# Kernel optimization log

Hardware: AMD Instinct MI355X
Metric: run time of the kernel (lower is better)

## Reference

```python
import jax, jax.numpy as jnp
import numpy as np

B, S, D = 1, 2048, 2048
H, DH, DHID, DKER = 16, 128, 128, 64
EPS = 1e-6

def _gelu(x):
    return jax.nn.gelu(x, approximate=False)  # torch F.gelu default is exact erf

def setup_inputs() -> dict:
    key = jax.random.key(0)
    ks = jax.random.split(key, 12)
    inp = {
        'q': jax.random.normal(ks[0], (B, S, D), jnp.float32),
        'k': jax.random.normal(ks[1], (B, S, D), jnp.float32),
        'v': jax.random.normal(ks[2], (B, S, D), jnp.float32),
        'lr_attn_mask': jax.random.randint(ks[3], (1, 1, S, S), 0, 2) > 0,
        'sparse_norms_lse': jax.random.normal(ks[4], (B, H, S, 1), jnp.float32),
        'sparse_attn_weights': jax.random.normal(ks[5], (B, H, S, S), jnp.float32) * 0.1,
        'kernel_q_mat1': jax.random.normal(ks[6], (H, DH, DHID), jnp.float32) * 0.05,
        'kernel_k_mat1': jax.random.normal(ks[7], (H, DH, DHID), jnp.float32) * 0.05,
        'kernel_q_mat2': jax.random.normal(ks[8], (H, DHID, DKER), jnp.float32) * 0.05,
        'kernel_k_mat2': jax.random.normal(ks[9], (H, DHID, DKER), jnp.float32) * 0.05,
        'interaction_k': jax.random.normal(ks[10], (H, DKER, DKER), jnp.float32) * 0.05,
        'scalingD': jnp.ones((1, H, 1, DKER), jnp.float32) * 1e-4,
        'scalingD2': jnp.ones((1, H, 1, DKER), jnp.float32) * 1e-4,
    }
    return inp

def reference(q, k, v, lr_attn_mask, sparse_norms_lse, sparse_attn_weights,
              kernel_q_mat1, kernel_k_mat1, kernel_q_mat2, kernel_k_mat2,
              interaction_k, scalingD, scalingD2):
    b, s, d = q.shape
    dh = d // H
    # [B,S,D] -> [B,H,S,dh]
    q = q.reshape(b, s, H, dh).transpose(0, 2, 1, 3)
    k = k.reshape(b, s, H, dh).transpose(0, 2, 1, 3)
    v = v.reshape(b, s, H, dh).transpose(0, 2, 1, 3)
    # per-head kernel feature maps (dropout is identity, p=0.0)
    q = _gelu(jnp.einsum('bhsd,hde->bhse', q, kernel_q_mat1))
    q = _gelu(jnp.einsum('bhsd,hde->bhse', q, kernel_q_mat2))
    k = _gelu(jnp.einsum('bhsd,hde->bhse', k, kernel_k_mat1))
    k = jnp.abs(scalingD) * _gelu(jnp.einsum('bhsd,hde->bhse', k, kernel_k_mat2))
    k = k + jnp.einsum('bhse,hef->bhsf', k, interaction_k) * scalingD2
    # low-rank kernelized scores: [B,H,S,S]
    out = jnp.einsum('bhse,bhte->bhst', jnp.abs(q), jnp.abs(k))
    mask = lr_attn_mask  # bool, broadcasts over [B,H,S,S]
    out = jnp.where(mask, out, 0.0)
    lr_norms_lse = jnp.log(out.sum(axis=-1, keepdims=True) + EPS)
    norm_factor_lse = jnp.logaddexp(lr_norms_lse, sparse_norms_lse)
    # log-domain merge of low-rank and sparse scores
    out = jnp.where(mask, jnp.log(out + EPS), sparse_attn_weights)
    out = jnp.exp(out - norm_factor_lse)
    out = jnp.einsum('bhst,bhtd->bhsd', out, v)
    return out.transpose(0, 2, 1, 3).reshape(b, s, d)
```

## Files before the change

kernel.cpp:

```cpp
#include <hip/hip_runtime.h>
#include <math.h>

#define S 2048
#define DD 2048
#define NH 16
#define DH 128
#define DHID 128
#define DKER 64
#define EPSF 1e-6f

typedef __attribute__((ext_vector_type(8))) short bf16x8;
typedef __attribute__((ext_vector_type(4))) float f32x4;

__device__ __forceinline__ float gelu_f(float x) {
    return 0.5f * x * (1.0f + erff(x * 0.7071067811865475f));
}

__device__ __forceinline__ ushort f2b(float x) {
    uint32_t u = __float_as_uint(x);
    uint32_t r = (u + 0x7FFFu + ((u >> 16) & 1u)) >> 16;
    return (ushort)r;
}

__global__ __launch_bounds__(256) void k_mlp1(const float* __restrict__ X,
                                              const float* __restrict__ Wall,
                                              float* __restrict__ Y) {
    const int h = blockIdx.y;
    const int s0 = blockIdx.x * 64;
    const int tid = threadIdx.x;
    const int ty = tid >> 4, tx = tid & 15;
    __shared__ float Xs[64][20];
    __shared__ float Ws[16][128];
    const float* Wh = Wall + h * DH * DHID;
    float acc[4][8] = {};

    const int lr = tid >> 2, lc = tid & 3;
    const int wr = tid >> 5, wc = tid & 31;
    for (int kc = 0; kc < 8; ++kc) {
        *(float4*)(&Xs[lr][lc * 4]) =
            *(const float4*)(X + (size_t)(s0 + lr) * DD + h * DH + kc * 16 + lc * 4);
        *(float4*)(&Ws[wr][wc * 4]) =
            *(const float4*)(Wh + (kc * 16 + wr) * DHID + wc * 4);
        *(float4*)(&Ws[wr + 8][wc * 4]) =
            *(const float4*)(Wh + (kc * 16 + wr + 8) * DHID + wc * 4);
        __syncthreads();
        #pragma unroll
        for (int kk = 0; kk < 16; ++kk) {
            float a[4];
            #pragma unroll
            for (int i = 0; i < 4; ++i) a[i] = Xs[ty * 4 + i][kk];
            float4 b0 = *(const float4*)(&Ws[kk][tx * 8]);
            float4 b1 = *(const float4*)(&Ws[kk][tx * 8 + 4]);
            #pragma unroll
            for (int i = 0; i < 4; ++i) {
                acc[i][0] += a[i] * b0.x; acc[i][1] += a[i] * b0.y;
                acc[i][2] += a[i] * b0.z; acc[i][3] += a[i] * b0.w;
                acc[i][4] += a[i] * b1.x; acc[i][5] += a[i] * b1.y;
                acc[i][6] += a[i] * b1.z; acc[i][7] += a[i] * b1.w;
            }
        }
        __syncthreads();
    }
    float* Yp = Y + ((size_t)h * S + s0) * DHID;
    #pragma unroll
    for (int i = 0; i < 4; ++i) {
        float4 o0, o1;
        o0.x = gelu_f(acc[i][0]); o0.y = gelu_f(acc[i][1]);
        o0.z = gelu_f(acc[i][2]); o0.w = gelu_f(acc[i][3]);
        o1.x = gelu_f(acc[i][4]); o1.y = gelu_f(acc[i][5]);
        o1.z = gelu_f(acc[i][6]); o1.w = gelu_f(acc[i][7]);
        *(float4*)(Yp + (ty * 4 + i) * DHID + tx * 8) = o0;
        *(float4*)(Yp + (ty * 4 + i) * DHID + tx * 8 + 4) = o1;
    }
}

__global__ __launch_bounds__(256) void k_mlp2_q(const float* __restrict__ Y1,
                                                const float* __restrict__ Wall,
                                                ushort* __restrict__ Q2) {
    const int h = blockIdx.y;
    const int s0 = blockIdx.x * 64;
    const int tid = threadIdx.x;
    const int ty = tid >> 4, tx = tid & 15;
    __shared__ float Ys[64][20];
    __shared__ float Ws[16][64];
    const float* Wh = Wall + h * DHID * DKER;
    float acc[4][4] = {};
    const int lr = tid >> 2, lc = tid & 3;
    const int wr = tid >> 4, wc = tid & 15;
    for (int kc = 0; kc < 8; ++kc) {
        *(float4*)(&Ys[lr][lc * 4]) =
            *(const float4*)(Y1 + ((size_t)h * S + s0 + lr) * DHID + kc * 16 + lc * 4);
        *(float4*)(&Ws[wr][wc * 4]) =
            *(const float4*)(Wh + (kc * 16 + wr) * DKER + wc * 4);
        __syncthreads();
        #pragma unroll
        for (int kk = 0; kk < 16; ++kk) {
            float4 b = *(const float4*)(&Ws[kk][tx * 4]);
            #pragma unroll
            for (int i = 0; i < 4; ++i) {
                float a = Ys[ty * 4 + i][kk];
                acc[i][0] += a * b.x; acc[i][1] += a * b.y;
                acc[i][2] += a * b.z; acc[i][3] += a * b.w;
            }
        }
        __syncthreads();
    }
    ushort* Qp = Q2 + ((size_t)h * S + s0) * DKER;
    #pragma unroll
    for (int i = 0; i < 4; ++i) {
        ushort4 o;
        o.x = f2b(fabsf(gelu_f(acc[i][0]))); o.y = f2b(fabsf(gelu_f(acc[i][1])));
        o.z = f2b(fabsf(gelu_f(acc[i][2]))); o.w = f2b(fabsf(gelu_f(acc[i][3])));
        *(ushort4*)(Qp + (ty * 4 + i) * DKER + tx * 4) = o;
    }
}

__global__ __launch_bounds__(256) void k_mlp2_k(const float* __restrict__ Y1,
                                                const float* __restrict__ Wall,
                                                const float* __restrict__ Ikall,
                                                const float* __restrict__ sD,
                                                const float* __restrict__ sD2,
                                                ushort* __restrict__ K3) {
    const int h = blockIdx.y;
    const int s0 = blockIdx.x * 64;
    const int tid = threadIdx.x;
    const int ty = tid >> 4, tx = tid & 15;
    __shared__ float Ys[64][20];
    __shared__ float Ws[16][64];
    __shared__ float K2s[64][68];
    __shared__ float Iks[64][64];
    const float* Wh = Wall + h * DHID * DKER;
    const float* Ikh = Ikall + h * DKER * DKER;
    #pragma unroll
    for (int it = 0; it < 4; ++it) {
        int idx = it * 256 + tid;
        int r = idx >> 4, c = idx & 15;
        *(float4*)(&Iks[r][c * 4]) = *(const float4*)(Ikh + r * DKER + c * 4);
    }
    float acc[4][4] = {};
    const int lr = tid >> 2, lc = tid & 3;
    const int wr = tid >> 4, wc = tid & 15;
    for (int kc = 0; kc < 8; ++kc) {
        *(float4*)(&Ys[lr][lc * 4]) =
            *(const float4*)(Y1 + ((size_t)h * S + s0 + lr) * DHID + kc * 16 + lc * 4);
        *(float4*)(&Ws[wr][wc * 4]) =
            *(const float4*)(Wh + (kc * 16 + wr) * DKER + wc * 4);
        __syncthreads();
        #pragma unroll
        for (int kk = 0; kk < 16; ++kk) {
            float4 b = *(const float4*)(&Ws[kk][tx * 4]);
            #pragma unroll
            for (int i = 0; i < 4; ++i) {
                float a = Ys[ty * 4 + i][kk];
                acc[i][0] += a * b.x; acc[i][1] += a * b.y;
                acc[i][2] += a * b.z; acc[i][3] += a * b.w;
            }
        }
        __syncthreads();
    }
    float sdv[4], sd2v[4];
    #pragma unroll
    for (int j = 0; j < 4; ++j) {
        sdv[j] = fabsf(sD[h * DKER + tx * 4 + j]);
        sd2v[j] = sD2[h * DKER + tx * 4 + j];
    }
    float k2r[4][4];
    #pragma unroll
    for (int i = 0; i < 4; ++i) {
        #pragma unroll
        for (int j = 0; j < 4; ++j) k2r[i][j] = sdv[j] * gelu_f(acc[i][j]);
        float4 o; o.x = k2r[i][0]; o.y = k2r[i][1]; o.z = k2r[i][2]; o.w = k2r[i][3];
        *(float4*)(&K2s[ty * 4 + i][tx * 4]) = o;
    }
    __syncthreads();
    float acc2[4][4] = {};
    #pragma unroll 16
    for (int f = 0; f < 64; ++f) {
        float4 b = *(const float4*)(&Iks[f][tx * 4]);
        #pragma unroll
        for (int i = 0; i < 4; ++i) {
            float a = K2s[ty * 4 + i][f];
            acc2[i][0] += a * b.x; acc2[i][1] += a * b.y;
            acc2[i][2] += a * b.z; acc2[i][3] += a * b.w;
        }
    }
    ushort* Kp = K3 + ((size_t)h * S + s0) * DKER;
    #pragma unroll
    for (int i = 0; i < 4; ++i) {
        ushort4 o;
        o.x = f2b(fabsf(k2r[i][0] + acc2[i][0] * sd2v[0]));
        o.y = f2b(fabsf(k2r[i][1] + acc2[i][1] * sd2v[1]));
        o.z = f2b(fabsf(k2r[i][2] + acc2[i][2] * sd2v[2]));
        o.w = f2b(fabsf(k2r[i][3] + acc2[i][3] * sd2v[3]));
        *(ushort4*)(Kp + (ty * 4 + i) * DKER + tx * 4) = o;
    }
}

__global__ __launch_bounds__(256) void k_vt(const float* __restrict__ V,
                                            ushort* __restrict__ Vt) {
    const int h = blockIdx.y;
    const int t0 = blockIdx.x * 64;
    const int tid = threadIdx.x;
    __shared__ ushort Ls[128][72];
    #pragma unroll
    for (int it = 0; it < 8; ++it) {
        int idx = it * 256 + tid;
        int r = idx >> 5, c4 = idx & 31;
        float4 v = *(const float4*)(V + (size_t)(t0 + r) * DD + h * DH + c4 * 4);
        Ls[c4 * 4 + 0][r] = f2b(v.x);
        Ls[c4 * 4 + 1][r] = f2b(v.y);
        Ls[c4 * 4 + 2][r] = f2b(v.z);
        Ls[c4 * 4 + 3][r] = f2b(v.w);
    }
    __syncthreads();
    #pragma unroll
    for (int it = 0; it < 4; ++it) {
        int idx = it * 256 + tid;
        int row = idx >> 3, cc = idx & 7;
        *(bf16x8*)(Vt + ((size_t)h * DH + row) * S + t0 + cc * 8) =
            *(const bf16x8*)(&Ls[row][cc * 8]);
    }
}

__global__ __launch_bounds__(256) void k_attn(const ushort* __restrict__ Q2,
                                              const ushort* __restrict__ K3,
                                              const ushort* __restrict__ Vt,
                                              const int* __restrict__ mask,
                                              const float* __restrict__ Wsp,
                                              const float* __restrict__ lse,
                                              float* __restrict__ out) {
    const int h = blockIdx.y;
    const int s0 = blockIdx.x * 64;
    const int tid = threadIdx.x;
    const int wv = tid >> 6;
    const int lane = tid & 63;
    const int ln = lane & 15;
    const int quad = lane >> 4;
    __shared__ ushort Q2s[64][72];
    __shared__ ushort K3s[64][72];
    __shared__ ushort Vts[128][72];
    __shared__ ushort Ps[4][16][72];

    #pragma unroll
    for (int it = 0; it < 2; ++it) {
        int idx = it * 256 + tid;
        int r = idx >> 3, c = idx & 7;
        *(bf16x8*)&Q2s[r][c * 8] =
            *(const bf16x8*)(Q2 + ((size_t)h * S + s0 + r) * DKER + c * 8);
    }

    f32x4 O[8];
    #pragma unroll
    for (int v = 0; v < 8; ++v) O[v] = (f32x4){0.f, 0.f, 0.f, 0.f};
    float rs[4] = {0.f, 0.f, 0.f, 0.f};
    const int srow_q = s0 + wv * 16 + quad * 4;

    for (int t0 = 0; t0 < S; t0 += 64) {
        __syncthreads();
        #pragma unroll
        for (int it = 0; it < 2; ++it) {
            int idx = it * 256 + tid;
            int r = idx >> 3, c = idx & 7;
            *(bf16x8*)&K3s[r][c * 8] =
                *(const bf16x8*)(K3 + ((size_t)h * S + t0 + r) * DKER + c * 8);
        }
        #pragma unroll
        for (int it = 0; it < 4; ++it) {
            int idx = it * 256 + tid;
            int r = idx >> 3, c = idx & 7;
            *(bf16x8*)&Vts[r][c * 8] =
                *(const bf16x8*)(Vt + ((size_t)h * DH + r) * S + t0 + c * 8);
        }
        int mk[4][4];
        float ww[4][4];
        #pragma unroll
        for (int n = 0; n < 4; ++n)
            #pragma unroll
            for (int r = 0; r < 4; ++r) {
                size_t off = (size_t)(srow_q + r) * S + t0 + n * 16 + ln;
                mk[n][r] = mask[off];
                ww[n][r] = Wsp[(size_t)h * S * S + off];
            }
        __syncthreads();

        f32x4 sc[4];
        #pragma unroll
        for (int n = 0; n < 4; ++n) sc[n] = (f32x4){0.f, 0.f, 0.f, 0.f};
        #pragma unroll
        for (int ks = 0; ks < 2; ++ks) {
            bf16x8 af = *(const bf16x8*)&Q2s[wv * 16 + ln][ks * 32 + quad * 8];
            #pragma unroll
            for (int n = 0; n < 4; ++n) {
                bf16x8 bf = *(const bf16x8*)&K3s[n * 16 + ln][ks * 32 + quad * 8];
                sc[n] = __builtin_amdgcn_mfma_f32_16x16x32_bf16(af, bf, sc[n], 0, 0, 0);
            }
        }
        #pragma unroll
        for (int n = 0; n < 4; ++n)
            #pragma unroll
            for (int r = 0; r < 4; ++r) {
                float s = sc[n][r];
                float p;
                if (mk[n][r]) { rs[r] += s; p = s + EPSF; }
                else          { p = expf(ww[n][r]); }
                Ps[wv][quad * 4 + r][n * 16 + ln] = f2b(p);
            }
        #pragma unroll
        for (int ks = 0; ks < 2; ++ks) {
            bf16x8 pf = *(const bf16x8*)&Ps[wv][ln][ks * 32 + quad * 8];
            #pragma unroll
            for (int v = 0; v < 8; ++v) {
                bf16x8 vf = *(const bf16x8*)&Vts[v * 16 + ln][ks * 32 + quad * 8];
                O[v] = __builtin_amdgcn_mfma_f32_16x16x32_bf16(pf, vf, O[v], 0, 0, 0);
            }
        }
    }
    #pragma unroll
    for (int r = 0; r < 4; ++r) {
        float v = rs[r];
        v += __shfl_xor(v, 1); v += __shfl_xor(v, 2);
        v += __shfl_xor(v, 4); v += __shfl_xor(v, 8);
        rs[r] = v;
    }
    float idv[4];
    #pragma unroll
    for (int r = 0; r < 4; ++r)
        idv[r] = 1.f / (rs[r] + EPSF + expf(lse[(size_t)h * S + srow_q + r]));
    #pragma unroll
    for (int v = 0; v < 8; ++v)
        #pragma unroll
        for (int r = 0; r < 4; ++r)
            out[(size_t)(srow_q + r) * DD + h * DH + v * 16 + ln] = O[v][r] * idv[r];
}

extern "C" void kernel_launch(void* const* d_in, const int* in_sizes, int n_in,
                              void* d_out, int out_size, void* d_ws, size_t ws_size,
                              hipStream_t stream) {
    const float* q   = (const float*)d_in[0];
    const float* k   = (const float*)d_in[1];
    const float* v   = (const float*)d_in[2];
    const int*   msk = (const int*)d_in[3];
    const float* lse = (const float*)d_in[4];
    const float* spw = (const float*)d_in[5];
    const float* wq1 = (const float*)d_in[6];
    const float* wk1 = (const float*)d_in[7];
    const float* wq2 = (const float*)d_in[8];
    const float* wk2 = (const float*)d_in[9];
    const float* ik  = (const float*)d_in[10];
    const float* sD  = (const float*)d_in[11];
    const float* sD2 = (const float*)d_in[12];
    float* out = (float*)d_out;

    float* ws = (float*)d_ws;
    float*  q1  = ws;
    float*  k1  = q1 + (size_t)NH * S * DHID;
    ushort* q2b = (ushort*)(k1 + (size_t)NH * S * DHID);
    ushort* k3b = q2b + (size_t)NH * S * DKER;
    ushort* vt  = k3b + (size_t)NH * S * DKER;

    dim3 g(S / 64, NH), b(256);
    k_mlp1<<<g, b, 0, stream>>>(q, wq1, q1);
    k_mlp1<<<g, b, 0, stream>>>(k, wk1, k1);
    k_mlp2_q<<<g, b, 0, stream>>>(q1, wq2, q2b);
    k_mlp2_k<<<g, b, 0, stream>>>(k1, wk2, ik, sD, sD2, k3b);
    k_vt<<<g, b, 0, stream>>>(v, vt);
    k_attn<<<g, b, 0, stream>>>(q2b, k3b, vt, msk, spw, lse, out);
}
```

Before: 564.9 us.

## Move feature MLPs to bf16 MFMA, bit-pack mask, split attention over keys

Replaces the fp32 SIMT feature-map GEMMs with fused bf16 MFMA kernels that keep the hidden layer in LDS, using weights transposed and converted in a small prep kernel. The int32 mask is packed into bitmasks with a ballot, which cuts mask traffic in the attention loop. Attention is split in two along the key dimension to get more blocks in flight, with a combine kernel that adds the partial sums and normalises. It also switches to the fast __expf. Running the MLPs in bf16 adds rounding error, and the split writes partial outputs to a workspace buffer.

```diff
diff --git a/kernel.cpp b/kernel.cpp
--- a/kernel.cpp
+++ b/kernel.cpp
@@ -22,178 +22,192 @@
     return (ushort)r;
 }
 
-__global__ __launch_bounds__(256) void k_mlp1(const float* __restrict__ X,
-                                              const float* __restrict__ Wall,
-                                              float* __restrict__ Y) {
+__device__ __forceinline__ bf16x8 pack8(float4 a, float4 b) {
+    bf16x8 r;
+    r[0] = (short)f2b(a.x); r[1] = (short)f2b(a.y);
+    r[2] = (short)f2b(a.z); r[3] = (short)f2b(a.w);
+    r[4] = (short)f2b(b.x); r[5] = (short)f2b(b.y);
+    r[6] = (short)f2b(b.z); r[7] = (short)f2b(b.w);
+    return r;
+}
+
+__global__ __launch_bounds__(256) void k_wprep(const float* __restrict__ wq1,
+                                               const float* __restrict__ wk1,
+                                               const float* __restrict__ wq2,
+                                               const float* __restrict__ wk2,
+                                               const float* __restrict__ ik,
+                                               ushort* __restrict__ w1qt,
+                                               ushort* __restrict__ w1kt,
+                                               ushort* __restrict__ w2qt,
+                                               ushort* __restrict__ w2kt,
+                                               ushort* __restrict__ ikt) {
+    const int h = blockIdx.x, m = blockIdx.y, tid = threadIdx.x;
+    const float* src; ushort* dst; int E, D;
+    if (m == 0)      { src = wq1 + h * 16384; dst = w1qt + h * 16384; E = 128; D = 128; }
+    else if (m == 1) { src = wk1 + h * 16384; dst = w1kt + h * 16384; E = 128; D = 128; }
+    else if (m == 2) { src = wq2 + h * 8192;  dst = w2qt + h * 8192;  E = 64;  D = 128; }
+    else if (m == 3) { src = wk2 + h * 8192;  dst = w2kt + h * 8192;  E = 64;  D = 128; }
+    else             { src = ik  + h * 4096;  dst = ikt  + h * 4096;  E = 64;  D = 64;  }
+    const int dsh = (D == 128) ? 7 : 6;
+    const int n = E * D;
+    for (int idx = tid; idx < n; idx += 256) {
+        int e = idx >> dsh, d = idx & (D - 1);
+        dst[idx] = f2b(src[d * E + e]);
+    }
+}
+
+__global__ __launch_bounds__(256) void k_fq(const float* __restrict__ X,
+                                            const ushort* __restrict__ w1t,
+                                            const ushort* __restrict__ w2t,
+                                            ushort* __restrict__ Q2) {
     const int h = blockIdx.y;
     const int s0 = blockIdx.x * 64;
     const int tid = threadIdx.x;
-    const int ty = tid >> 4, tx = tid & 15;
-    __shared__ float Xs[64][20];
-    __shared__ float Ws[16][128];
-    const float* Wh = Wall + h * DH * DHID;
-    float acc[4][8] = {};
-
-    const int lr = tid >> 2, lc = tid & 3;
-    const int wr = tid >> 5, wc = tid & 31;
-    for (int kc = 0; kc < 8; ++kc) {
-        *(float4*)(&Xs[lr][lc * 4]) =
-            *(const float4*)(X + (size_t)(s0 + lr) * DD + h * DH + kc * 16 + lc * 4);
-        *(float4*)(&Ws[wr][wc * 4]) =
-            *(const float4*)(Wh + (kc * 16 + wr) * DHID + wc * 4);
-        *(float4*)(&Ws[wr + 8][wc * 4]) =
-            *(const float4*)(Wh + (kc * 16 + wr + 8) * DHID + wc * 4);
-        __syncthreads();
-        #pragma unroll
-        for (int kk = 0; kk < 16; ++kk) {
-            float a[4];
-            #pragma unroll
-            for (int i = 0; i < 4; ++i) a[i] = Xs[ty * 4 + i][kk];
-            float4 b0 = *(const float4*)(&Ws[kk][tx * 8]);
-            float4 b1 = *(const float4*)(&Ws[kk][tx * 8 + 4]);
-            #pragma unroll
-            for (int i = 0; i < 4; ++i) {
-                acc[i][0] += a[i] * b0.x; acc[i][1] += a[i] * b0.y;
-                acc[i][2] += a[i] * b0.z; acc[i][3] += a[i] * b0.w;
-                acc[i][4] += a[i] * b1.x; acc[i][5] += a[i] * b1.y;
-                acc[i][6] += a[i] * b1.z; acc[i][7] += a[i] * b1.w;
-            }
-        }
-        __syncthreads();
-    }
-    float* Yp = Y + ((size_t)h * S + s0) * DHID;
-    #pragma unroll
-    for (int i = 0; i < 4; ++i) {
-        float4 o0, o1;
-        o0.x = gelu_f(acc[i][0]); o0.y = gelu_f(acc[i][1]);
-        o0.z = gelu_f(acc[i][2]); o0.w = gelu_f(acc[i][3]);
-        o1.x = gelu_f(acc[i][4]); o1.y = gelu_f(acc[i][5]);
-        o1.z = gelu_f(acc[i][6]); o1.w = gelu_f(acc[i][7]);
-        *(float4*)(Yp + (ty * 4 + i) * DHID + tx * 8) = o0;
-        *(float4*)(Yp + (ty * 4 + i) * DHID + tx * 8 + 4) = o1;
-    }
-}
-
-__global__ __launch_bounds__(256) void k_mlp2_q(const float* __restrict__ Y1,
-                                                const float* __restrict__ Wall,
-                                                ushort* __restrict__ Q2) {
+    const int wv = tid >> 6, lane = tid & 63;
+    const int ln = lane & 15, quad = lane >> 4;
+    __shared__ ushort Y1s[64][136];
+
+    const float* Xr = X + (size_t)(s0 + wv * 16 + ln) * DD + h * DH;
+    bf16x8 a1[4];
+    #pragma unroll
+    for (int ks = 0; ks < 4; ++ks)
+        a1[ks] = pack8(*(const float4*)(Xr + ks * 32 + quad * 8),
+                       *(const float4*)(Xr + ks * 32 + quad * 8 + 4));
+
+    const ushort* W1h = w1t + (size_t)h * DH * DHID;
+    f32x4 c1[8];
+    #pragma unroll
+    for (int n = 0; n < 8; ++n) c1[n] = (f32x4){0.f, 0.f, 0.f, 0.f};
+    #pragma unroll
+    for (int n = 0; n < 8; ++n)
+        #pragma unroll
+        for (int ks = 0; ks < 4; ++ks) {
+            bf16x8 b = *(const bf16x8*)(W1h + (size_t)(n * 16 + ln) * DHID +
+                                        ks * 32 + quad * 8);
+            c1[n] = __builtin_amdgcn_mfma_f32_16x16x32_bf16(a1[ks], b, c1[n], 0, 0, 0);
+        }
+    #pragma unroll
+    for (int n = 0; n < 8; ++n)
+        #pragma unroll
+        for (int r = 0; r < 4; ++r)
+            Y1s[wv * 16 + quad * 4 + r][n * 16 + ln] = f2b(gelu_f(c1[n][r]));
+
+    bf16x8 a2[4];
+    #pragma unroll
+    for (int ks = 0; ks < 4; ++ks)
+        a2[ks] = *(const bf16x8*)&Y1s[wv * 16 + ln][ks * 32 + quad * 8];
+    const ushort* W2h = w2t + (size_t)h * DKER * DHID;
+    f32x4 c2[4];
+    #pragma unroll
+    for (int n = 0; n < 4; ++n) c2[n] = (f32x4){0.f, 0.f, 0.f, 0.f};
+    #pragma unroll
+    for (int n = 0; n < 4; ++n)
+        #pragma unroll
+        for (int ks = 0; ks < 4; ++ks) {
+            bf16x8 b = *(const bf16x8*)(W2h + (size_t)(n * 16 + ln) * DHID +
+                                        ks * 32 + quad * 8);
+            c2[n] = __builtin_amdgcn_mfma_f32_16x16x32_bf16(a2[ks], b, c2[n], 0, 0, 0);
+        }
+    #pragma unroll
+    for (int n = 0; n < 4; ++n)
+        #pragma unroll
+        for (int r = 0; r < 4; ++r)
+            Q2[((size_t)h * S + s0 + wv * 16 + quad * 4 + r) * DKER + n * 16 + ln] =
+                f2b(fabsf(gelu_f(c2[n][r])));
+}
+
+__global__ __launch_bounds__(256) void k_fk(const float* __restrict__ X,
+                                            const ushort* __restrict__ w1t,
+                                            const ushort* __restrict__ w2t,
+                                            const ushort* __restrict__ ikt,
+                                            const float* __restrict__ sD,
+                                            const float* __restrict__ sD2,
+                                            ushort* __restrict__ K3) {
     const int h = blockIdx.y;
     const int s0 = blockIdx.x * 64;
     const int tid = threadIdx.x;
-    const int ty = tid >> 4, tx = tid & 15;
-    __shared__ float Ys[64][20];
-    __shared__ float Ws[16][64];
-    const float* Wh = Wall + h * DHID * DKER;
-    float acc[4][4] = {};
-    const int lr = tid >> 2, lc = tid & 3;
-    const int wr = tid >> 4, wc = tid & 15;
-    for (int kc = 0; kc < 8; ++kc) {
-        *(float4*)(&Ys[lr][lc * 4]) =
-            *(const float4*)(Y1 + ((size_t)h * S + s0 + lr) * DHID + kc * 16 + lc * 4);
-        *(float4*)(&Ws[wr][wc * 4]) =
-            *(const float4*)(Wh + (kc * 16 + wr) * DKER + wc * 4);
-        __syncthreads();
-        #pragma unroll
-        for (int kk = 0; kk < 16; ++kk) {
-            float4 b = *(const float4*)(&Ws[kk][tx * 4]);
-            #pragma unroll
-            for (int i = 0; i < 4; ++i) {
-                float a = Ys[ty * 4 + i][kk];
-                acc[i][0] += a * b.x; acc[i][1] += a * b.y;
-                acc[i][2] += a * b.z; acc[i][3] += a * b.w;
-            }
-        }
-        __syncthreads();
-    }
-    ushort* Qp = Q2 + ((size_t)h * S + s0) * DKER;
-    #pragma unroll
-    for (int i = 0; i < 4; ++i) {
-        ushort4 o;
-        o.x = f2b(fabsf(gelu_f(acc[i][0]))); o.y = f2b(fabsf(gelu_f(acc[i][1])));
-        o.z = f2b(fabsf(gelu_f(acc[i][2]))); o.w = f2b(fabsf(gelu_f(acc[i][3])));
-        *(ushort4*)(Qp + (ty * 4 + i) * DKER + tx * 4) = o;
-    }
-}
-
-__global__ __launch_bounds__(256) void k_mlp2_k(const float* __restrict__ Y1,
-                                                const float* __restrict__ Wall,
-                                                const float* __restrict__ Ikall,
-                                                const float* __restrict__ sD,
-                                                const float* __restrict__ sD2,
-                                                ushort* __restrict__ K3) {
-    const int h = blockIdx.y;
-    const int s0 = blockIdx.x * 64;
-    const int tid = threadIdx.x;
-    const int ty = tid >> 4, tx = tid & 15;
-    __shared__ float Ys[64][20];
-    __shared__ float Ws[16][64];
-    __shared__ float K2s[64][68];
-    __shared__ float Iks[64][64];
-    const float* Wh = Wall + h * DHID * DKER;
-    const float* Ikh = Ikall + h * DKER * DKER;
-    #pragma unroll
-    for (int it = 0; it < 4; ++it) {
-        int idx = it * 256 + tid;
-        int r = idx >> 4, c = idx & 15;
-        *(float4*)(&Iks[r][c * 4]) = *(const float4*)(Ikh + r * DKER + c * 4);
-    }
-    float acc[4][4] = {};
-    const int lr = tid >> 2, lc = tid & 3;
-    const int wr = tid >> 4, wc = tid & 15;
-    for (int kc = 0; kc < 8; ++kc) {
-        *(float4*)(&Ys[lr][lc * 4]) =
-            *(const float4*)(Y1 + ((size_t)h * S + s0 + lr) * DHID + kc * 16 + lc * 4);
-        *(float4*)(&Ws[wr][wc * 4]) =
-            *(const float4*)(Wh + (kc * 16 + wr) * DKER + wc * 4);
-        __syncthreads();
-        #pragma unroll
-        for (int kk = 0; kk < 16; ++kk) {
-            float4 b = *(const float4*)(&Ws[kk][tx * 4]);
-            #pragma unroll
-            for (int i = 0; i < 4; ++i) {
-                float a = Ys[ty * 4 + i][kk];
-                acc[i][0] += a * b.x; acc[i][1] += a * b.y;
-                acc[i][2] += a * b.z; acc[i][3] += a * b.w;
-            }
-        }
-        __syncthreads();
-    }
+    const int wv = tid >> 6, lane = tid & 63;
+    const int ln = lane & 15, quad = lane >> 4;
+    __shared__ ushort Y1s[64][136];
+    __shared__ ushort K2s[64][72];
+
+    const float* Xr = X + (size_t)(s0 + wv * 16 + ln) * DD + h * DH;
+    bf16x8 a1[4];
+    #pragma unroll
+    for (int ks = 0; ks < 4; ++ks)
+        a1[ks] = pack8(*(const float4*)(Xr + ks * 32 + quad * 8),
+                       *(const float4*)(Xr + ks * 32 + quad * 8 + 4));
+
+    const ushort* W1h = w1t + (size_t)h * DH * DHID;
+    f32x4 c1[8];
+    #pragma unroll
+    for (int n = 0; n < 8; ++n) c1[n] = (f32x4){0.f, 0.f, 0.f, 0.f};
+    #pragma unroll
+    for (int n = 0; n < 8; ++n)
+        #pragma unroll
+        for (int ks = 0; ks < 4; ++ks) {
+            bf16x8 b = *(const bf16x8*)(W1h + (size_t)(n * 16 + ln) * DHID +
+                                        ks * 32 + quad * 8);
+            c1[n] = __builtin_amdgcn_mfma_f32_16x16x32_bf16(a1[ks], b, c1[n], 0, 0, 0);
+        }
+    #pragma unroll
+    for (int n = 0; n < 8; ++n)
+        #pragma unroll
+        for (int r = 0; r < 4; ++r)
+            Y1s[wv * 16 + quad * 4 + r][n * 16 + ln] = f2b(gelu_f(c1[n][r]));
+
+    bf16x8 a2[4];
+    #pragma unroll
+    for (int ks = 0; ks < 4; ++ks)
+        a2[ks] = *(const bf16x8*)&Y1s[wv * 16 + ln][ks * 32 + quad * 8];
+    const ushort* W2h = w2t + (size_t)h * DKER * DHID;
+    f32x4 c2[4];
+    #pragma unroll
+    for (int n = 0; n < 4; ++n) c2[n] = (f32x4){0.f, 0.f, 0.f, 0.f};
+    #pragma unroll
+    for (int n = 0; n < 4; ++n)
+        #pragma unroll
+        for (int ks = 0; ks < 4; ++ks) {
+            bf16x8 b = *(const bf16x8*)(W2h + (size_t)(n * 16 + ln) * DHID +
+                                        ks * 32 + quad * 8);
+            c2[n] = __builtin_amdgcn_mfma_f32_16x16x32_bf16(a2[ks], b, c2[n], 0, 0, 0);
+        }
+    float k2v[4][4];
     float sdv[4], sd2v[4];
     #pragma unroll
-    for (int j = 0; j < 4; ++j) {
-        sdv[j] = fabsf(sD[h * DKER + tx * 4 + j]);
-        sd2v[j] = sD2[h * DKER + tx * 4 + j];
-    }
-    float k2r[4][4];
-    #pragma unroll
-    for (int i = 0; i < 4; ++i) {
-        #pragma unroll
-        for (int j = 0; j < 4; ++j) k2r[i][j] = sdv[j] * gelu_f(acc[i][j]);
-        float4 o; o.x = k2r[i][0]; o.y = k2r[i][1]; o.z = k2r[i][2]; o.w = k2r[i][3];
-        *(float4*)(&K2s[ty * 4 + i][tx * 4]) = o;
-    }
-    __syncthreads();
-    float acc2[4][4] = {};
-    #pragma unroll 16
-    for (int f = 0; f < 64; ++f) {
-        float4 b = *(const float4*)(&Iks[f][tx * 4]);
-        #pragma unroll
-        for (int i = 0; i < 4; ++i) {
-            float a = K2s[ty * 4 + i][f];
-            acc2[i][0] += a * b.x; acc2[i][1] += a * b.y;
-            acc2[i][2] += a * b.z; acc2[i][3] += a * b.w;
-        }
-    }
-    ushort* Kp = K3 + ((size_t)h * S + s0) * DKER;
-    #pragma unroll
-    for (int i = 0; i < 4; ++i) {
-        ushort4 o;
-        o.x = f2b(fabsf(k2r[i][0] + acc2[i][0] * sd2v[0]));
-        o.y = f2b(fabsf(k2r[i][1] + acc2[i][1] * sd2v[1]));
-        o.z = f2b(fabsf(k2r[i][2] + acc2[i][2] * sd2v[2]));
-        o.w = f2b(fabsf(k2r[i][3] + acc2[i][3] * sd2v[3]));
-        *(ushort4*)(Kp + (ty * 4 + i) * DKER + tx * 4) = o;
-    }
+    for (int n = 0; n < 4; ++n) {
+        sdv[n]  = fabsf(sD[h * DKER + n * 16 + ln]);
+        sd2v[n] = sD2[h * DKER + n * 16 + ln];
+    }
+    #pragma unroll
+    for (int n = 0; n < 4; ++n)
+        #pragma unroll
+        for (int r = 0; r < 4; ++r) {
+            k2v[n][r] = sdv[n] * gelu_f(c2[n][r]);
+            K2s[wv * 16 + quad * 4 + r][n * 16 + ln] = f2b(k2v[n][r]);
+        }
+    bf16x8 a3[2];
+    #pragma unroll
+    for (int ks = 0; ks < 2; ++ks)
+        a3[ks] = *(const bf16x8*)&K2s[wv * 16 + ln][ks * 32 + quad * 8];
+    const ushort* Ikh = ikt + (size_t)h * DKER * DKER;
+    f32x4 c3[4];
+    #pragma unroll
+    for (int n = 0; n < 4; ++n) c3[n] = (f32x4){0.f, 0.f, 0.f, 0.f};
+    #pragma unroll
+    for (int n = 0; n < 4; ++n)
+        #pragma unroll
+        for (int ks = 0; ks < 2; ++ks) {
+            bf16x8 b = *(const bf16x8*)(Ikh + (size_t)(n * 16 + ln) * DKER +
+                                        ks * 32 + quad * 8);
+            c3[n] = __builtin_amdgcn_mfma_f32_16x16x32_bf16(a3[ks], b, c3[n], 0, 0, 0);
+        }
+    #pragma unroll
+    for (int n = 0; n < 4; ++n)
+        #pragma unroll
+        for (int r = 0; r < 4; ++r)
+            K3[((size_t)h * S + s0 + wv * 16 + quad * 4 + r) * DKER + n * 16 + ln] =
+                f2b(fabsf(k2v[n][r] + c3[n][r] * sd2v[n]));
 }
 
 __global__ __launch_bounds__(256) void k_vt(const float* __restrict__ V,
@@ -222,87 +236,101 @@
     }
 }
 
-__global__ __launch_bounds__(256) void k_attn(const ushort* __restrict__ Q2,
-                                              const ushort* __restrict__ K3,
-                                              const ushort* __restrict__ Vt,
-                                              const int* __restrict__ mask,
-                                              const float* __restrict__ Wsp,
-                                              const float* __restrict__ lse,
-                                              float* __restrict__ out) {
+__global__ __launch_bounds__(256) void k_mpack(const int* __restrict__ mask,
+                                               uint* __restrict__ pm) {
+    const int gw = blockIdx.x * 4 + (threadIdx.x >> 6);
+    const int lane = threadIdx.x & 63;
+    const int row = gw >> 5;
+    const int w64 = gw & 31;
+    int mv = mask[(size_t)row * S + w64 * 64 + lane];
+    unsigned long long b = __ballot(mv != 0);
+    if (lane == 0)  pm[row * 64 + w64 * 2]     = (uint)b;
+    if (lane == 32) pm[row * 64 + w64 * 2 + 1] = (uint)(b >> 32);
+}
+
+__global__ __launch_bounds__(256, 4) void k_attn(const ushort* __restrict__ Q2,
+                                                 const ushort* __restrict__ K3,
+                                                 const ushort* __restrict__ Vt,
+                                                 const uint* __restrict__ pm,
+                                                 const float* __restrict__ Wsp,
+                                                 float* __restrict__ Op,
+                                                 float* __restrict__ rsp) {
     const int h = blockIdx.y;
     const int s0 = blockIdx.x * 64;
+    const int z = blockIdx.z;
+    const int tbase = z * (S / 2);
     const int tid = threadIdx.x;
-    const int wv = tid >> 6;
-    const int lane = tid & 63;
-    const int ln = lane & 15;
-    const int quad = lane >> 4;
-    __shared__ ushort Q2s[64][72];
+    const int wv = tid >> 6, lane = tid & 63;
+    const int ln = lane & 15, quad = lane >> 4;
     __shared__ ushort K3s[64][72];
     __shared__ ushort Vts[128][72];
     __shared__ ushort Ps[4][16][72];
 
-    #pragma unroll
-    for (int it = 0; it < 2; ++it) {
-        int idx = it * 256 + tid;
-        int r = idx >> 3, c = idx & 7;
-        *(bf16x8*)&Q2s[r][c * 8] =
-            *(const bf16x8*)(Q2 + ((size_t)h * S + s0 + r) * DKER + c * 8);
-    }
+    const ushort* K3h = K3 + (size_t)h * S * DKER;
+    const ushort* Vth = Vt + (size_t)h * DH * S;
+    const float*  Wh  = Wsp + (size_t)h * S * S;
+    const int srow_q = s0 + wv * 16 + quad * 4;
+
+    bf16x8 aq[2];
+    #pragma unroll
+    for (int ks = 0; ks < 2; ++ks)
+        aq[ks] = *(const bf16x8*)(Q2 + ((size_t)h * S + s0 + wv * 16 + ln) * DKER +
+                                  ks * 32 + quad * 8);
 
     f32x4 O[8];
     #pragma unroll
     for (int v = 0; v < 8; ++v) O[v] = (f32x4){0.f, 0.f, 0.f, 0.f};
     float rs[4] = {0.f, 0.f, 0.f, 0.f};
-    const int srow_q = s0 + wv * 16 + quad * 4;
-
-    for (int t0 = 0; t0 < S; t0 += 64) {
+
+    for (int it = 0; it < 16; ++it) {
+        const int t0 = tbase + it * 64;
         __syncthreads();
         #pragma unroll
-        for (int it = 0; it < 2; ++it) {
-            int idx = it * 256 + tid;
-            int r = idx >> 3, c = idx & 7;
-            *(bf16x8*)&K3s[r][c * 8] =
-                *(const bf16x8*)(K3 + ((size_t)h * S + t0 + r) * DKER + c * 8);
-        }
-        #pragma unroll
-        for (int it = 0; it < 4; ++it) {
-            int idx = it * 256 + tid;
-            int r = idx >> 3, c = idx & 7;
-            *(bf16x8*)&Vts[r][c * 8] =
-                *(const bf16x8*)(Vt + ((size_t)h * DH + r) * S + t0 + c * 8);
-        }
-        int mk[4][4];
+        for (int c = 0; c < 2; ++c) {
+            int idx = c * 256 + tid;
+            int r = idx >> 3, cc = idx & 7;
+            *(bf16x8*)&K3s[r][cc * 8] =
+                *(const bf16x8*)(K3h + (size_t)(t0 + r) * DKER + cc * 8);
+        }
+        #pragma unroll
+        for (int c = 0; c < 4; ++c) {
+            int idx = c * 256 + tid;
+            int r = idx >> 3, cc = idx & 7;
+            *(bf16x8*)&Vts[r][cc * 8] =
+                *(const bf16x8*)(Vth + (size_t)r * S + t0 + cc * 8);
+        }
+        __syncthreads();
+        uint2 mw[4];
+        #pragma unroll
+        for (int r = 0; r < 4; ++r)
+            mw[r] = *(const uint2*)(pm + (size_t)(srow_q + r) * 64 + (t0 >> 5));
         float ww[4][4];
+        #pragma unroll
+        for (int n = 0; n < 4; ++n)
+            #pragma unroll
+            for (int r = 0; r < 4; ++r)
+                ww[n][r] = Wh[(size_t)(srow_q + r) * S + t0 + n * 16 + ln];
+
+        f32x4 sc[4];
+        #pragma unroll
+        for (int n = 0; n < 4; ++n) sc[n] = (f32x4){0.f, 0.f, 0.f, 0.f};
+        #pragma unroll
+        for (int ks = 0; ks < 2; ++ks)
+            #pragma unroll
+            for (int n = 0; n < 4; ++n) {
+                bf16x8 bf = *(const bf16x8*)&K3s[n * 16 + ln][ks * 32 + quad * 8];
+                sc[n] = __builtin_amdgcn_mfma_f32_16x16x32_bf16(aq[ks], bf, sc[n], 0, 0, 0);
+            }
         #pragma unroll
         for (int n = 0; n < 4; ++n)
             #pragma unroll
             for (int r = 0; r < 4; ++r) {
-                size_t off = (size_t)(srow_q + r) * S + t0 + n * 16 + ln;
-                mk[n][r] = mask[off];
-                ww[n][r] = Wsp[(size_t)h * S * S + off];
-            }
-        __syncthreads();
-
-        f32x4 sc[4];
-        #pragma unroll
-        for (int n = 0; n < 4; ++n) sc[n] = (f32x4){0.f, 0.f, 0.f, 0.f};
-        #pragma unroll
-        for (int ks = 0; ks < 2; ++ks) {
-            bf16x8 af = *(const bf16x8*)&Q2s[wv * 16 + ln][ks * 32 + quad * 8];
-            #pragma unroll
-            for (int n = 0; n < 4; ++n) {
-                bf16x8 bf = *(const bf16x8*)&K3s[n * 16 + ln][ks * 32 + quad * 8];
-                sc[n] = __builtin_amdgcn_mfma_f32_16x16x32_bf16(af, bf, sc[n], 0, 0, 0);
-            }
-        }
-        #pragma unroll
-        for (int n = 0; n < 4; ++n)
-            #pragma unroll
-            for (int r = 0; r < 4; ++r) {
+                uint word = (n >= 2) ? mw[r].y : mw[r].x;
+                int m = (word >> (((n & 1) << 4) + ln)) & 1;
                 float s = sc[n][r];
                 float p;
-                if (mk[n][r]) { rs[r] += s; p = s + EPSF; }
-                else          { p = expf(ww[n][r]); }
+                if (m) { rs[r] += s; p = s + EPSF; }
+                else   { p = __expf(ww[n][r]); }
                 Ps[wv][quad * 4 + r][n * 16 + ln] = f2b(p);
             }
         #pragma unroll
@@ -322,15 +350,38 @@
         v += __shfl_xor(v, 4); v += __shfl_xor(v, 8);
         rs[r] = v;
     }
-    float idv[4];
-    #pragma unroll
-    for (int r = 0; r < 4; ++r)
-        idv[r] = 1.f / (rs[r] + EPSF + expf(lse[(size_t)h * S + srow_q + r]));
+    if (ln == 0) {
+        #pragma unroll
+        for (int r = 0; r < 4; ++r)
+            rsp[((size_t)z * NH + h) * S + srow_q + r] = rs[r];
+    }
     #pragma unroll
     for (int v = 0; v < 8; ++v)
         #pragma unroll
         for (int r = 0; r < 4; ++r)
-            out[(size_t)(srow_q + r) * DD + h * DH + v * 16 + ln] = O[v][r] * idv[r];
+            Op[(((size_t)z * NH + h) * S + srow_q + r) * DH + v * 16 + ln] = O[v][r];
+}
+
+__global__ __launch_bounds__(256) void k_comb(const float* __restrict__ Op,
+                                              const float* __restrict__ rsp,
+                                              const float* __restrict__ lse,
+                                              float* __restrict__ out) {
+    const int h = blockIdx.y;
+    const int s0 = blockIdx.x * 64;
+    const int tid = threadIdx.x;
+    const int c = (tid & 31) * 4;
+    const int r0 = tid >> 5;
+    for (int rr = r0; rr < 64; rr += 8) {
+        const int row = s0 + rr;
+        float rs = rsp[(size_t)h * S + row] + rsp[((size_t)NH + h) * S + row];
+        float idv = 1.f / (rs + EPSF + expf(lse[(size_t)h * S + row]));
+        float4 a = *(const float4*)(Op + ((size_t)h * S + row) * DH + c);
+        float4 b = *(const float4*)(Op + (((size_t)NH + h) * S + row) * DH + c);
+        float4 o;
+        o.x = (a.x + b.x) * idv; o.y = (a.y + b.y) * idv;
+        o.z = (a.z + b.z) * idv; o.w = (a.w + b.w) * idv;
+        *(float4*)(out + (size_t)row * DD + h * DH + c) = o;
+    }
 }
 
 extern "C" void kernel_launch(void* const* d_in, const int* in_sizes, int n_in,
@@ -351,18 +402,25 @@
     const float* sD2 = (const float*)d_in[12];
     float* out = (float*)d_out;
 
-    float* ws = (float*)d_ws;
-    float*  q1  = ws;
-    float*  k1  = q1 + (size_t)NH * S * DHID;
-    ushort* q2b = (ushort*)(k1 + (size_t)NH * S * DHID);
-    ushort* k3b = q2b + (size_t)NH * S * DKER;
-    ushort* vt  = k3b + (size_t)NH * S * DKER;
+    ushort* q2b  = (ushort*)d_ws;
+    ushort* k3b  = q2b + (size_t)NH * S * DKER;
+    ushort* vt   = k3b + (size_t)NH * S * DKER;
+    uint*   pm   = (uint*)(vt + (size_t)NH * DH * S);
+    ushort* w1qt = (ushort*)(pm + (size_t)S * 64);
+    ushort* w1kt = w1qt + (size_t)NH * DH * DHID;
+    ushort* w2qt = w1kt + (size_t)NH * DH * DHID;
+    ushort* w2kt = w2qt + (size_t)NH * DKER * DHID;
+    ushort* ikt  = w2kt + (size_t)NH * DKER * DHID;
+    float*  Op   = (float*)(ikt + (size_t)NH * DKER * DKER);
+    float*  rsp  = Op + (size_t)2 * NH * S * DH;
 
     dim3 g(S / 64, NH), b(256);
-    k_mlp1<<<g, b, 0, stream>>>(q, wq1, q1);
-    k_mlp1<<<g, b, 0, stream>>>(k, wk1, k1);
-    k_mlp2_q<<<g, b, 0, stream>>>(q1, wq2, q2b);
-    k_mlp2_k<<<g, b, 0, stream>>>(k1, wk2, ik, sD, sD2, k3b);
+    k_wprep<<<dim3(NH, 5), b, 0, stream>>>(wq1, wk1, wq2, wk2, ik,
+                                           w1qt, w1kt, w2qt, w2kt, ikt);
+    k_mpack<<<dim3(S * 32 / 4), b, 0, stream>>>(msk, pm);
     k_vt<<<g, b, 0, stream>>>(v, vt);
-    k_attn<<<g, b, 0, stream>>>(q2b, k3b, vt, msk, spw, lse, out);
-}
+    k_fq<<<g, b, 0, stream>>>(q, w1qt, w2qt, q2b);
+    k_fk<<<g, b, 0, stream>>>(k, w1kt, w2kt, ikt, sD, sD2, k3b);
+    k_attn<<<dim3(S / 64, NH, 2), b, 0, stream>>>(q2b, k3b, vt, pm, spw, Op, rsp);
+    k_comb<<<g, b, 0, stream>>>(Op, rsp, lse, out);
+}
```

After: 515.8 us. -8.7%, faster.
